# Kernel optimization log

Measured on AMD Instinct MI355X. Metric: run time of the kernel, lower is better.

The kernel has to match this reference:

```python
import jax, jax.numpy as jnp
import numpy as np

D_MODEL = 2048
D_STATE = 16
D_CONV = 4
EXPAND = 2
D_INNER = EXPAND * D_MODEL  # 4096
DT_RANK = 128               # ceil(2048/16)
BATCH = 2
SEQ = 1024


def setup_inputs() -> dict:
    key = jax.random.key(0)
    ks = jax.random.split(key, 10)
    n = lambda k, shape, scale: jax.random.normal(k, shape, dtype=jnp.float32) * scale
    # A_log = log(arange(1..N)) broadcast over channels, exactly as in the torch init
    A_log = jnp.log(jnp.tile(jnp.arange(1, D_STATE + 1, dtype=jnp.float32)[None, :], (D_INNER, 1)))
    return {
        "hidden_states": n(ks[0], (BATCH, SEQ, D_MODEL), 1.0),
        "W_in": n(ks[1], (2 * D_INNER, D_MODEL), 0.02),
        "conv_w": n(ks[2], (D_INNER, D_CONV), 0.2),
        "conv_b": n(ks[3], (D_INNER,), 0.02),
        "W_x": n(ks[4], (DT_RANK + 2 * D_STATE, D_INNER), 0.02),
        "W_dt": n(ks[5], (D_INNER, DT_RANK), 0.05),
        "b_dt": n(ks[6], (D_INNER,), 0.5) - 4.0,  # softplus(b_dt) ~ small dt, like inv-softplus init
        "A_log": A_log,
        "D_skip": jnp.ones((D_INNER,), jnp.float32),
        "W_out": n(ks[7], (D_MODEL, D_INNER), 0.02),
    }


def _mamba_forward(hidden_states, W_in, conv_w, conv_b, W_x, W_dt, b_dt, A_log, D_skip, W_out):
    B, L, _ = hidden_states.shape
    # in_proj then split into x (SSM path) and z (gate)
    xz = hidden_states @ W_in.T                      # (B, L, 2*Di)
    x, z = jnp.split(xz, 2, axis=-1)                 # (B, L, Di) each
    # causal depthwise conv1d (kernel D_CONV, left pad D_CONV-1) + SiLU
    xp = jnp.pad(x, ((0, 0), (D_CONV - 1, 0), (0, 0)))
    xc = conv_b
    for k in range(D_CONV):
        xc = xc + conv_w[:, k] * xp[:, k:k + L, :]
    x = jax.nn.silu(xc)                              # (B, L, Di)
    # input-dependent dt, B, C
    x_dbl = x @ W_x.T                                # (B, L, dt_rank + 2N)
    dt_low, B_in, C_in = jnp.split(x_dbl, [DT_RANK, DT_RANK + D_STATE], axis=-1)
    dt = dt_low @ W_dt.T                             # (B, L, Di); bias added inside scan (delta_bias)
    delta = jax.nn.softplus(dt + b_dt)               # (B, L, Di)
    A = -jnp.exp(A_log)                              # (Di, N)

    def step(h, inp):
        delta_t, u_t, B_t, C_t = inp                 # (B,Di),(B,Di),(B,N),(B,N)
        dA = jnp.exp(delta_t[..., None] * A)         # (B, Di, N)
        h = dA * h + (delta_t * u_t)[..., None] * B_t[:, None, :]
        y_t = jnp.einsum('bdn,bn->bd', h, C_t)
        return h, y_t

    h0 = jnp.zeros((B, D_INNER, D_STATE), x.dtype)
    xs = (jnp.swapaxes(delta, 0, 1), jnp.swapaxes(x, 0, 1),
          jnp.swapaxes(B_in, 0, 1), jnp.swapaxes(C_in, 0, 1))
    _, ys = jax.lax.scan(step, h0, xs)               # ys: (L, B, Di)
    y = jnp.swapaxes(ys, 0, 1)                       # (B, L, Di)
    y = y + D_skip * x                               # skip connection
    y = y * jax.nn.silu(z)                           # output gating
    return y @ W_out.T                               # (B, L, D_MODEL)


def reference(hidden_states, W_in, conv_w, conv_b, W_x, W_dt, b_dt, A_log, D_skip, W_out):
    return _mamba_forward(hidden_states, W_in, conv_w, conv_b, W_x, W_dt, b_dt, A_log, D_skip, W_out)
```

## Files before the change

### kernel.cpp

```cpp
#include <hip/hip_runtime.h>
#include <hip/hip_bf16.h>


#define BATCH 2
#define SEQ 1024
#define DMODEL 2048
#define DINNER 4096
#define DSTATE 16
#define DTRANK 128
#define ROWS (BATCH * SEQ)
#define XDBL_N (DTRANK + 2 * DSTATE)
#define NCHUNK 32
#define LOG2_NCHUNK 5
#define CLEN (SEQ / NCHUNK)
#define WXPAD 192
#define SPLITK 16

typedef unsigned short ushort_t;
typedef __attribute__((ext_vector_type(8))) short short8;
typedef __attribute__((ext_vector_type(4))) float f32x4;

__device__ __forceinline__ ushort_t bf16_rne(float f) {
  unsigned u = __float_as_uint(f);
  return (ushort_t)((u + 0x7FFFu + ((u >> 16) & 1u)) >> 16);
}

__global__ __launch_bounds__(256) void cast_bf16(
    const float* __restrict__ x, ushort_t* __restrict__ o, int n4) {
  int i = blockIdx.x * 256 + threadIdx.x;
  if (i >= n4) return;
  float4 v = ((const float4*)x)[i];
  ushort4 h;
  h.x = bf16_rne(v.x); h.y = bf16_rne(v.y);
  h.z = bf16_rne(v.z); h.w = bf16_rne(v.w);
  ((ushort4*)o)[i] = h;
}

__global__ __launch_bounds__(256) void cast_wx(
    const float* __restrict__ wx, ushort_t* __restrict__ o) {
  int i = blockIdx.x * 256 + threadIdx.x;
  if (i >= WXPAD * (DINNER / 4)) return;
  int row = i >> 10;
  ushort4 h = {0, 0, 0, 0};
  if (row < XDBL_N) {
    float4 v = ((const float4*)wx)[i];
    h.x = bf16_rne(v.x); h.y = bf16_rne(v.y);
    h.z = bf16_rne(v.z); h.w = bf16_rne(v.w);
  }
  ((ushort4*)o)[i] = h;
}

template <int TM, int TN, int EPI, bool SK>
__global__ __launch_bounds__(256, 2) void gemm_bf16(
    const ushort_t* __restrict__ X, int lda,
    const ushort_t* __restrict__ W, int ldb,
    const float* __restrict__ bias,
    float* __restrict__ C, int ldc, int kslice, size_t sstride) {
  constexpr int MI = TM / 32;
  constexpr int NI = TN / 32;
  constexpr int G = (TM + TN) / 32;
  __shared__ __attribute__((aligned(16))) ushort_t lds[(TM + TN) * 64];

  const int tid = threadIdx.x;
  const int lane = tid & 63;
  const int w = tid >> 6;
  const int wm = w & 1, wn = w >> 1;
  const int m0 = blockIdx.x * TM;
  const int n0 = blockIdx.y * TN;
  const int kbase = SK ? blockIdx.z * kslice : 0;

  const int lrow = lane >> 3;
  const int csw = (lane & 7) ^ lrow;
  const int quad = lane >> 4;
  const int l15 = lane & 15;
  const int x0 = quad ^ (lane & 7);
  const int baseA = (wm * (TM / 2) + l15) * 64;
  const int baseB = (TM + wn * (TN / 2) + l15) * 64;

  f32x4 acc[MI][NI] = {};

  for (int kt = 0; kt < kslice; kt += 64) {
#pragma unroll
    for (int j = 0; j < G; j++) {
      const int r0 = (w * G + j) * 8;
      const int row = r0 + lrow;
      const ushort_t* src = (r0 < TM)
          ? X + (size_t)(m0 + row) * lda + kbase + kt + csw * 8
          : W + (size_t)(n0 + row - TM) * ldb + kbase + kt + csw * 8;
      __builtin_amdgcn_global_load_lds(
          (const __attribute__((address_space(1))) unsigned int*)src,
          (__attribute__((address_space(3))) unsigned int*)&lds[r0 * 64],
          16, 0, 0);
    }
    __syncthreads();

#pragma unroll
    for (int ks = 0; ks < 2; ks++) {
      const int xo = (x0 ^ (ks * 4)) * 8;
      short8 a[MI], b[NI];
#pragma unroll
      for (int mi = 0; mi < MI; mi++)
        a[mi] = *(const short8*)&lds[baseA + mi * 1024 + xo];
#pragma unroll
      for (int ni = 0; ni < NI; ni++)
        b[ni] = *(const short8*)&lds[baseB + ni * 1024 + xo];
#pragma unroll
      for (int mi = 0; mi < MI; mi++)
#pragma unroll
        for (int ni = 0; ni < NI; ni++)
          acc[mi][ni] = __builtin_amdgcn_mfma_f32_16x16x32_bf16(
              a[mi], b[ni], acc[mi][ni], 0, 0, 0);
    }
    __syncthreads();
  }

  float* Cs = SK ? (C + (size_t)blockIdx.z * sstride) : C;
#pragma unroll
  for (int mi = 0; mi < MI; mi++)
#pragma unroll
    for (int ni = 0; ni < NI; ni++) {
      int row = m0 + wm * (TM / 2) + mi * 16 + quad * 4;
      int col = n0 + wn * (TN / 2) + ni * 16 + l15;
#pragma unroll
      for (int r = 0; r < 4; r++) {
        float v = acc[mi][ni][r];
        if (EPI == 1) {
          v += bias[col];
          v = (v > 20.f) ? v : log1pf(__expf(v));
        }
        Cs[(size_t)(row + r) * ldc + col] = v;
      }
    }
}

__device__ __forceinline__ void bar() {
  asm volatile("" ::: "memory");
  __builtin_amdgcn_s_barrier();
  asm volatile("" ::: "memory");
}
#define VMWAIT(n) asm volatile("s_waitcnt vmcnt(" #n ")" ::: "memory")

#define CLUSTER(AF, BF, MH, NH)                                           \
  do {                                                                    \
    __builtin_amdgcn_s_setprio(1);                                        \
    _Pragma("unroll")                                                     \
    for (int mi = 0; mi < 4; mi++)                                        \
      _Pragma("unroll")                                                   \
      for (int ni = 0; ni < 2; ni++)                                      \
        _Pragma("unroll")                                                 \
        for (int ks = 0; ks < 2; ks++)                                    \
          acc[(MH) * 4 + mi][(NH) * 2 + ni] =                             \
              __builtin_amdgcn_mfma_f32_16x16x32_bf16(                    \
                  AF[mi][ks], BF[ni][ks],                                 \
                  acc[(MH) * 4 + mi][(NH) * 2 + ni], 0, 0, 0);            \
    __builtin_amdgcn_s_setprio(0);                                        \
  } while (0)

__global__ __launch_bounds__(512, 2) void gemm256(
    const ushort_t* __restrict__ X, int lda,
    const ushort_t* __restrict__ W, int ldb,
    float* __restrict__ C, int ldc, int K) {
  __shared__ __attribute__((aligned(16))) ushort_t lds[65536];
  const int tid = threadIdx.x;
  const int lane = tid & 63;
  const int w = tid >> 6;
  const int wm = w >> 2, wn = w & 3;
  const int m0 = blockIdx.x * 256;
  const int n0 = blockIdx.y * 256;
  const int lrow = lane >> 3;
  const int csw = (lane & 7) ^ lrow;
  const int quad = lane >> 4;
  const int l15 = lane & 15;
  const int sx = lane & 7;

  f32x4 acc[8][4] = {};
  short8 a[4][2], b0[2][2], b1[2][2];

  const ushort_t* Asrc = X + (size_t)(m0 + w * 8 + lrow) * lda + csw * 8;
  const ushort_t* Bsrc = W + (size_t)(n0 + w * 8 + lrow) * ldb + csw * 8;

  auto stA = [&](int buf, int g, int kt) {
    __builtin_amdgcn_global_load_lds(
        (const __attribute__((address_space(1))) unsigned int*)
            (Asrc + (size_t)g * 64 * lda + kt),
        (__attribute__((address_space(3))) unsigned int*)
            &lds[buf * 16384 + (g * 64 + w * 8) * 64],
        16, 0, 0);
  };
  auto stB = [&](int buf, int g, int kt) {
    __builtin_amdgcn_global_load_lds(
        (const __attribute__((address_space(1))) unsigned int*)
            (Bsrc + (size_t)g * 64 * ldb + kt),
        (__attribute__((address_space(3))) unsigned int*)
            &lds[32768 + buf * 16384 + (g * 64 + w * 8) * 64],
        16, 0, 0);
  };
  auto rdA = [&](int buf, int half, int mi, int ks) {
    int row = wm * 128 + half * 64 + mi * 16 + l15;
    int ch = (ks * 4 + quad) ^ sx;
    return *(const short8*)&lds[buf * 16384 + row * 64 + ch * 8];
  };
  auto rdB = [&](int buf, int nh, int ni, int ks) {
    int row = wn * 64 + nh * 32 + ni * 16 + l15;
    int ch = (ks * 4 + quad) ^ sx;
    return *(const short8*)&lds[32768 + buf * 16384 + row * 64 + ch * 8];
  };

#pragma unroll
  for (int g = 0; g < 4; g++) stA(0, g, 0);
#pragma unroll
  for (int g = 0; g < 4; g++) stB(0, g, 0);
  VMWAIT(0);
  bar();

  const int NT = K / 64;
  int cur = 0;
  for (int t = 0; t < NT - 1; ++t) {
    const int nxt = cur ^ 1;
    const int k2 = (t + 1) * 64;
#pragma unroll
    for (int mi = 0; mi < 4; mi++)
#pragma unroll
      for (int ks = 0; ks < 2; ks++) a[mi][ks] = rdA(cur, 0, mi, ks);
#pragma unroll
    for (int ni = 0; ni < 2; ni++)
#pragma unroll
      for (int ks = 0; ks < 2; ks++) b0[ni][ks] = rdB(cur, 0, ni, ks);
    stB(nxt, 0, k2); stB(nxt, 1, k2);
    bar();
    CLUSTER(a, b0, 0, 0);
    bar();
#pragma unroll
    for (int ni = 0; ni < 2; ni++)
#pragma unroll
      for (int ks = 0; ks < 2; ks++) b1[ni][ks] = rdB(cur, 1, ni, ks);
    stB(nxt, 2, k2); stB(nxt, 3, k2);
    bar();
    CLUSTER(a, b1, 0, 1);
    VMWAIT(4);
    bar();
#pragma unroll
    for (int mi = 0; mi < 4; mi++)
#pragma unroll
      for (int ks = 0; ks < 2; ks++) a[mi][ks] = rdA(cur, 1, mi, ks);
    stA(nxt, 0, k2); stA(nxt, 2, k2);
    bar();
    CLUSTER(a, b1, 1, 1);
    bar();
    stA(nxt, 1, k2); stA(nxt, 3, k2);
    bar();
    CLUSTER(a, b0, 1, 0);
    VMWAIT(2);
    bar();
    cur = nxt;
  }
  {
#pragma unroll
    for (int mi = 0; mi < 4; mi++)
#pragma unroll
      for (int ks = 0; ks < 2; ks++) a[mi][ks] = rdA(cur, 0, mi, ks);
#pragma unroll
    for (int ni = 0; ni < 2; ni++)
#pragma unroll
      for (int ks = 0; ks < 2; ks++) b0[ni][ks] = rdB(cur, 0, ni, ks);
    bar();
    CLUSTER(a, b0, 0, 0);
    bar();
#pragma unroll
    for (int ni = 0; ni < 2; ni++)
#pragma unroll
      for (int ks = 0; ks < 2; ks++) b1[ni][ks] = rdB(cur, 1, ni, ks);
    bar();
    CLUSTER(a, b1, 0, 1);
    VMWAIT(0);
    bar();
#pragma unroll
    for (int mi = 0; mi < 4; mi++)
#pragma unroll
      for (int ks = 0; ks < 2; ks++) a[mi][ks] = rdA(cur, 1, mi, ks);
    bar();
    CLUSTER(a, b1, 1, 1);
    CLUSTER(a, b0, 1, 0);
  }

#pragma unroll
  for (int mi = 0; mi < 8; mi++)
#pragma unroll
    for (int ni = 0; ni < 4; ni++) {
      int row = m0 + wm * 128 + mi * 16 + quad * 4;
      int col = n0 + wn * 64 + ni * 16 + l15;
#pragma unroll
      for (int r = 0; r < 4; r++)
        C[(size_t)(row + r) * ldc + col] = acc[mi][ni][r];
    }
}

__global__ __launch_bounds__(192) void reduce_sk(
    const float* __restrict__ partials, float* __restrict__ xdbl,
    ushort_t* __restrict__ dtb) {
  int m = blockIdx.x;
  int c = threadIdx.x;
  if (c >= XDBL_N) return;
  float s = 0.f;
#pragma unroll
  for (int z = 0; z < SPLITK; z++)
    s += partials[(size_t)z * ROWS * WXPAD + (size_t)m * WXPAD + c];
  xdbl[(size_t)m * XDBL_N + c] = s;
  if (c < DTRANK) dtb[(size_t)m * DTRANK + c] = bf16_rne(s);
}

__global__ __launch_bounds__(256) void conv_silu(
    const float* __restrict__ xz, const float* __restrict__ cw,
    const float* __restrict__ cb, float* __restrict__ xs,
    ushort_t* __restrict__ xsb) {
  int idx = blockIdx.x * 256 + threadIdx.x;
  if (idx >= ROWS * DINNER / 4) return;
  int d4 = idx & (DINNER / 4 - 1);
  int bt = idx >> 10;
  int t = bt & (SEQ - 1);
  int d = d4 * 4;
  float4 c4 = *(const float4*)&cb[d];
  float wv[4][4];
  *(float4*)wv[0] = *(const float4*)&cw[(d + 0) * 4];
  *(float4*)wv[1] = *(const float4*)&cw[(d + 1) * 4];
  *(float4*)wv[2] = *(const float4*)&cw[(d + 2) * 4];
  *(float4*)wv[3] = *(const float4*)&cw[(d + 3) * 4];
  float a0 = c4.x, a1 = c4.y, a2 = c4.z, a3 = c4.w;
#pragma unroll
  for (int k = 0; k < 4; k++) {
    int tt = t - 3 + k;
    if (tt >= 0) {
      float4 v = *(const float4*)&xz[(size_t)(bt - 3 + k) * (2 * DINNER) + d];
      a0 += wv[0][k] * v.x;
      a1 += wv[1][k] * v.y;
      a2 += wv[2][k] * v.z;
      a3 += wv[3][k] * v.w;
    }
  }
  float4 s;
  s.x = a0 / (1.f + __expf(-a0));
  s.y = a1 / (1.f + __expf(-a1));
  s.z = a2 / (1.f + __expf(-a2));
  s.w = a3 / (1.f + __expf(-a3));
  *(float4*)&xs[(size_t)bt * DINNER + d] = s;
  ushort4 h;
  h.x = bf16_rne(s.x); h.y = bf16_rne(s.y);
  h.z = bf16_rne(s.z); h.w = bf16_rne(s.w);
  *(ushort4*)&xsb[(size_t)bt * DINNER + d] = h;
}

__global__ __launch_bounds__(256) void scan_pass1(
    const float* __restrict__ delta, const float* __restrict__ xs,
    const float* __restrict__ xdbl, const float* __restrict__ A_log,
    float* __restrict__ hpart, float* __restrict__ sumd) {
  int g = blockIdx.x * 256 + threadIdx.x;
  int d = g & (DINNER - 1);
  int rest = g >> 12;
  int c = rest & (NCHUNK - 1);
  int b = rest >> LOG2_NCHUNK;

  float Adn[16];
#pragma unroll
  for (int q = 0; q < 4; q++) {
    float4 a = *(const float4*)&A_log[d * 16 + q * 4];
    Adn[q * 4 + 0] = -__expf(a.x); Adn[q * 4 + 1] = -__expf(a.y);
    Adn[q * 4 + 2] = -__expf(a.z); Adn[q * 4 + 3] = -__expf(a.w);
  }

  float h[16] = {};
  float sd = 0.f;
  const size_t t0 = (size_t)b * SEQ + c * CLEN;
  const float* dp = delta + t0 * DINNER + d;
  const float* up = xs + t0 * DINNER + d;
  const float* xb = xdbl + t0 * XDBL_N + DTRANK;

  for (int i = 0; i < CLEN; i++) {
    float dt = dp[(size_t)i * DINNER];
    float u = up[(size_t)i * DINNER];
    sd += dt;
    float du = dt * u;
    float Bv[16];
#pragma unroll
    for (int q = 0; q < 4; q++)
      *(float4*)&Bv[q * 4] = *(const float4*)&xb[i * XDBL_N + q * 4];
#pragma unroll
    for (int n = 0; n < 16; n++)
      h[n] = __expf(dt * Adn[n]) * h[n] + du * Bv[n];
  }

  float* hp = hpart + ((size_t)(c * BATCH + b) * DINNER + d) * 16;
#pragma unroll
  for (int q = 0; q < 4; q++) *(float4*)&hp[q * 4] = *(const float4*)&h[q * 4];
  sumd[(size_t)(c * BATCH + b) * DINNER + d] = sd;
}

__global__ __launch_bounds__(256) void scan_pass2(
    float* __restrict__ hph, const float* __restrict__ sumd,
    const float* __restrict__ A_log) {
  int g = blockIdx.x * 256 + threadIdx.x;
  int n = g & 15;
  int d = (g >> 4) & (DINNER - 1);
  int b = g >> 16;

  float Adn = -__expf(A_log[d * 16 + n]);
  float h = 0.f;
  for (int c = 0; c < NCHUNK; c++) {
    size_t base = (size_t)(c * BATCH + b) * DINNER + d;
    float part = hph[base * 16 + n];
    hph[base * 16 + n] = h;
    h = __expf(Adn * sumd[base]) * h + part;
  }
}

__global__ __launch_bounds__(256) void scan_pass3(
    const float* __restrict__ xz, const float* __restrict__ xs,
    const float* __restrict__ xdbl, const float* __restrict__ A_log,
    const float* __restrict__ D_skip, const float* __restrict__ h0,
    const float* __restrict__ delta, ushort_t* __restrict__ gated) {
  int g = blockIdx.x * 256 + threadIdx.x;
  int d = g & (DINNER - 1);
  int rest = g >> 12;
  int c = rest & (NCHUNK - 1);
  int b = rest >> LOG2_NCHUNK;

  float Adn[16];
#pragma unroll
  for (int q = 0; q < 4; q++) {
    float4 a = *(const float4*)&A_log[d * 16 + q * 4];
    Adn[q * 4 + 0] = -__expf(a.x); Adn[q * 4 + 1] = -__expf(a.y);
    Adn[q * 4 + 2] = -__expf(a.z); Adn[q * 4 + 3] = -__expf(a.w);
  }
  float Dd = D_skip[d];

  float h[16];
  const float* hp = h0 + ((size_t)(c * BATCH + b) * DINNER + d) * 16;
#pragma unroll
  for (int q = 0; q < 4; q++) *(float4*)&h[q * 4] = *(const float4*)&hp[q * 4];

  const size_t t0 = (size_t)b * SEQ + c * CLEN;
  const float* dl = delta + t0 * DINNER + d;
  const float* up = xs + t0 * DINNER + d;
  const float* zb = xz + t0 * (2 * DINNER) + DINNER + d;
  const float* xb = xdbl + t0 * XDBL_N + DTRANK;
  ushort_t* gp = gated + t0 * DINNER + d;

  for (int i = 0; i < CLEN; i++) {
    float dt = dl[(size_t)i * DINNER];
    float u = up[(size_t)i * DINNER];
    float du = dt * u;
    float Bv[16], Cv[16];
#pragma unroll
    for (int q = 0; q < 4; q++) {
      *(float4*)&Bv[q * 4] = *(const float4*)&xb[i * XDBL_N + q * 4];
      *(float4*)&Cv[q * 4] = *(const float4*)&xb[i * XDBL_N + DSTATE + q * 4];
    }
    float y = 0.f;
#pragma unroll
    for (int n = 0; n < 16; n++) {
      h[n] = __expf(dt * Adn[n]) * h[n] + du * Bv[n];
      y += h[n] * Cv[n];
    }
    float z = zb[(size_t)i * (2 * DINNER)];
    float sz = z / (1.f + __expf(-z));
    gp[(size_t)i * DINNER] = bf16_rne((y + Dd * u) * sz);
  }
}

extern "C" void kernel_launch(void* const* d_in, const int* in_sizes, int n_in,
                              void* d_out, int out_size, void* d_ws, size_t ws_size,
                              hipStream_t stream) {
  const float* hidden = (const float*)d_in[0];
  const float* W_in   = (const float*)d_in[1];
  const float* conv_w = (const float*)d_in[2];
  const float* conv_b = (const float*)d_in[3];
  const float* W_x    = (const float*)d_in[4];
  const float* W_dt   = (const float*)d_in[5];
  const float* b_dt   = (const float*)d_in[6];
  const float* A_log  = (const float*)d_in[7];
  const float* D_skip = (const float*)d_in[8];
  const float* W_out  = (const float*)d_in[9];
  float* out = (float*)d_out;

  float* ws    = (float*)d_ws;
  float* xz    = ws;
  float* xs    = xz + (size_t)ROWS * 2 * DINNER;
  float* xdbl  = xs + (size_t)ROWS * DINNER;
  float* delta = xdbl + (size_t)ROWS * XDBL_N;
  float* sumd  = delta + (size_t)ROWS * DINNER;
  float* hph   = sumd + (size_t)BATCH * DINNER * NCHUNK;
  ushort_t* Hb   = (ushort_t*)(hph + (size_t)BATCH * DINNER * NCHUNK * DSTATE);
  ushort_t* Wb1  = Hb + (size_t)ROWS * DMODEL;
  ushort_t* Wxb  = Wb1 + (size_t)2 * DINNER * DMODEL;
  ushort_t* Wdtb = Wxb + (size_t)WXPAD * DINNER;
  ushort_t* xsb  = Wdtb + (size_t)DINNER * DTRANK;
  ushort_t* dtb  = xsb + (size_t)ROWS * DINNER;
  float* partials = (float*)Wb1;
  ushort_t* Woutb = Wb1;
  ushort_t* gatedb = Wb1 + (size_t)DMODEL * DINNER;

  dim3 blk(256);

  cast_bf16<<<(ROWS * DMODEL / 4 + 255) / 256, blk, 0, stream>>>(
      hidden, Hb, ROWS * DMODEL / 4);
  cast_bf16<<<(2 * DINNER * DMODEL / 4 + 255) / 256, blk, 0, stream>>>(
      W_in, Wb1, 2 * DINNER * DMODEL / 4);

  gemm256<<<dim3(8, 32), dim3(512), 0, stream>>>(
      Hb, DMODEL, Wb1, DMODEL, xz, 2 * DINNER, DMODEL);

  conv_silu<<<(ROWS * DINNER / 4 + 255) / 256, blk, 0, stream>>>(
      xz, conv_w, conv_b, xs, xsb);

  cast_wx<<<(WXPAD * DINNER / 4 + 255) / 256, blk, 0, stream>>>(W_x, Wxb);
  cast_bf16<<<(DINNER * DTRANK / 4 + 255) / 256, blk, 0, stream>>>(
      W_dt, Wdtb, DINNER * DTRANK / 4);

  gemm_bf16<128, 64, 0, true><<<dim3(16, 3, SPLITK), blk, 0, stream>>>(
      xsb, DINNER, Wxb, DINNER, nullptr, partials, WXPAD, DINNER / SPLITK,
      (size_t)ROWS * WXPAD);
  reduce_sk<<<ROWS, dim3(WXPAD), 0, stream>>>(partials, xdbl, dtb);

  gemm_bf16<128, 128, 1, false><<<dim3(16, 32), blk, 0, stream>>>(
      dtb, DTRANK, Wdtb, DTRANK, b_dt, delta, DINNER, DTRANK, 0);

  scan_pass1<<<(BATCH * DINNER * NCHUNK) / 256, blk, 0, stream>>>(
      delta, xs, xdbl, A_log, hph, sumd);
  scan_pass2<<<(BATCH * DINNER * DSTATE) / 256, blk, 0, stream>>>(
      hph, sumd, A_log);
  scan_pass3<<<(BATCH * DINNER * NCHUNK) / 256, blk, 0, stream>>>(
      xz, xs, xdbl, A_log, D_skip, hph, delta, gatedb);

  cast_bf16<<<(DMODEL * DINNER / 4 + 255) / 256, blk, 0, stream>>>(
      W_out, Woutb, DMODEL * DINNER / 4);

  gemm_bf16<128, 64, 0, false><<<dim3(16, 32), blk, 0, stream>>>(
      gatedb, DINNER, Woutb, DINNER, nullptr, out, DMODEL, DINNER, 0);
}
```

Measured before the change: 461.0 us.

## Swizzle GEMM block order for XCD locality and issue A prefetch earlier

Remaps block indices in gemm256 and two gemm_bf16 launches so that consecutive blocks, which are spread across XCDs, cover contiguous tile regions. This is meant to improve L2 reuse of shared operand tiles. In gemm256 the next-tile A loads are issued alongside the B loads earlier in each iteration, with explicit lgkmcnt waits and sched barriers before the MFMA clusters. This deepens prefetch overlap and drops one barrier per iteration, at the cost of more in-flight loads and possible scheduling rigidity.

Result: no change. 457.7 us (-0.7%).

```diff
diff --git a/kernel.cpp b/kernel.cpp
--- a/kernel.cpp
+++ b/kernel.cpp
@@ -50,7 +50,7 @@
   ((ushort4*)o)[i] = h;
 }
 
-template <int TM, int TN, int EPI, bool SK>
+template <int TM, int TN, int EPI, bool SK, bool SWZ>
 __global__ __launch_bounds__(256, 2) void gemm_bf16(
     const ushort_t* __restrict__ X, int lda,
     const ushort_t* __restrict__ W, int ldb,
@@ -65,8 +65,16 @@
   const int lane = tid & 63;
   const int w = tid >> 6;
   const int wm = w & 1, wn = w >> 1;
-  const int m0 = blockIdx.x * TM;
-  const int n0 = blockIdx.y * TN;
+  int bx = blockIdx.x, by = blockIdx.y;
+  if (SWZ) {
+    const int bid = by * 16 + bx;
+    const int cpx = (16 * gridDim.y) >> 3;
+    const int sz = (bid & 7) * cpx + (bid >> 3);
+    bx = sz & 15;
+    by = sz >> 4;
+  }
+  const int m0 = bx * TM;
+  const int n0 = by * TN;
   const int kbase = SK ? blockIdx.z * kslice : 0;
 
   const int lrow = lane >> 3;
@@ -139,6 +147,8 @@
   asm volatile("" ::: "memory");
 }
 #define VMWAIT(n) asm volatile("s_waitcnt vmcnt(" #n ")" ::: "memory")
+#define LGKM0 asm volatile("s_waitcnt lgkmcnt(0)" ::: "memory")
+#define SCHED0 __builtin_amdgcn_sched_barrier(0)
 
 #define CLUSTER(AF, BF, MH, NH)                                           \
   do {                                                                    \
@@ -165,8 +175,10 @@
   const int lane = tid & 63;
   const int w = tid >> 6;
   const int wm = w >> 2, wn = w & 3;
-  const int m0 = blockIdx.x * 256;
-  const int n0 = blockIdx.y * 256;
+  const int bid = blockIdx.y * 8 + blockIdx.x;
+  const int swz = (bid & 7) * 32 + (bid >> 3);
+  const int m0 = (swz & 7) * 256;
+  const int n0 = (swz >> 3) * 256;
   const int lrow = lane >> 3;
   const int csw = (lane & 7) ^ lrow;
   const int quad = lane >> 4;
@@ -226,28 +238,28 @@
     for (int ni = 0; ni < 2; ni++)
 #pragma unroll
       for (int ks = 0; ks < 2; ks++) b0[ni][ks] = rdB(cur, 0, ni, ks);
-    stB(nxt, 0, k2); stB(nxt, 1, k2);
-    bar();
+    stB(nxt, 0, k2); stB(nxt, 1, k2); stA(nxt, 0, k2); stA(nxt, 2, k2);
+    bar();
+    LGKM0; SCHED0;
     CLUSTER(a, b0, 0, 0);
     bar();
 #pragma unroll
     for (int ni = 0; ni < 2; ni++)
 #pragma unroll
       for (int ks = 0; ks < 2; ks++) b1[ni][ks] = rdB(cur, 1, ni, ks);
-    stB(nxt, 2, k2); stB(nxt, 3, k2);
-    bar();
+    stB(nxt, 2, k2); stB(nxt, 3, k2); stA(nxt, 1, k2); stA(nxt, 3, k2);
+    bar();
+    LGKM0; SCHED0;
     CLUSTER(a, b1, 0, 1);
-    VMWAIT(4);
+    VMWAIT(8);
     bar();
 #pragma unroll
     for (int mi = 0; mi < 4; mi++)
 #pragma unroll
       for (int ks = 0; ks < 2; ks++) a[mi][ks] = rdA(cur, 1, mi, ks);
-    stA(nxt, 0, k2); stA(nxt, 2, k2);
-    bar();
+    bar();
+    LGKM0; SCHED0;
     CLUSTER(a, b1, 1, 1);
-    bar();
-    stA(nxt, 1, k2); stA(nxt, 3, k2);
     bar();
     CLUSTER(a, b0, 1, 0);
     VMWAIT(2);
@@ -264,6 +276,7 @@
 #pragma unroll
       for (int ks = 0; ks < 2; ks++) b0[ni][ks] = rdB(cur, 0, ni, ks);
     bar();
+    LGKM0; SCHED0;
     CLUSTER(a, b0, 0, 0);
     bar();
 #pragma unroll
@@ -271,6 +284,7 @@
 #pragma unroll
       for (int ks = 0; ks < 2; ks++) b1[ni][ks] = rdB(cur, 1, ni, ks);
     bar();
+    LGKM0; SCHED0;
     CLUSTER(a, b1, 0, 1);
     VMWAIT(0);
     bar();
@@ -279,6 +293,7 @@
 #pragma unroll
       for (int ks = 0; ks < 2; ks++) a[mi][ks] = rdA(cur, 1, mi, ks);
     bar();
+    LGKM0; SCHED0;
     CLUSTER(a, b1, 1, 1);
     CLUSTER(a, b0, 1, 0);
   }
@@ -515,12 +530,12 @@
   cast_bf16<<<(DINNER * DTRANK / 4 + 255) / 256, blk, 0, stream>>>(
       W_dt, Wdtb, DINNER * DTRANK / 4);
 
-  gemm_bf16<128, 64, 0, true><<<dim3(16, 3, SPLITK), blk, 0, stream>>>(
+  gemm_bf16<128, 64, 0, true, false><<<dim3(16, 3, SPLITK), blk, 0, stream>>>(
       xsb, DINNER, Wxb, DINNER, nullptr, partials, WXPAD, DINNER / SPLITK,
       (size_t)ROWS * WXPAD);
   reduce_sk<<<ROWS, dim3(WXPAD), 0, stream>>>(partials, xdbl, dtb);
 
-  gemm_bf16<128, 128, 1, false><<<dim3(16, 32), blk, 0, stream>>>(
+  gemm_bf16<128, 128, 1, false, true><<<dim3(16, 32), blk, 0, stream>>>(
       dtb, DTRANK, Wdtb, DTRANK, b_dt, delta, DINNER, DTRANK, 0);
 
   scan_pass1<<<(BATCH * DINNER * NCHUNK) / 256, blk, 0, stream>>>(
@@ -533,6 +548,6 @@
   cast_bf16<<<(DMODEL * DINNER / 4 + 255) / 256, blk, 0, stream>>>(
       W_out, Woutb, DMODEL * DINNER / 4);
 
-  gemm_bf16<128, 64, 0, false><<<dim3(16, 32), blk, 0, stream>>>(
+  gemm_bf16<128, 64, 0, false, true><<<dim3(16, 32), blk, 0, stream>>>(
       gatedb, DINNER, Woutb, DINNER, nullptr, out, DMODEL, DINNER, 0);
 }
```
